# Optimization experiments

Hardware: AMD Instinct MI355X
Metric: run time of the kernel (lower is better)

The kernel has to match this reference:

```python
import jax, jax.numpy as jnp
import numpy as np

B, S, IN_DIM = 4, 2048, 16
D_MODEL, N_HEADS, D_FF = 256, 8, 512
HEAD_DIM = D_MODEL // N_HEADS
EPS = 1e-5


def setup_inputs() -> dict:
    key = jax.random.key(0)
    ks = jax.random.split(key, 16)
    s = 0.02
    return {
        "src": jax.random.normal(ks[0], (B, S, IN_DIM), dtype=jnp.float32),
        "We": jax.random.normal(ks[1], (IN_DIM, D_MODEL), dtype=jnp.float32) * s,
        "be": jnp.zeros((D_MODEL,), jnp.float32),
        "Wq": jax.random.normal(ks[2], (D_MODEL, D_MODEL), dtype=jnp.float32) * s,
        "bq": jnp.zeros((D_MODEL,), jnp.float32),
        "Wk": jax.random.normal(ks[3], (D_MODEL, D_MODEL), dtype=jnp.float32) * s,
        "bk": jnp.zeros((D_MODEL,), jnp.float32),
        "Wv": jax.random.normal(ks[4], (D_MODEL, D_MODEL), dtype=jnp.float32) * s,
        "bv": jnp.zeros((D_MODEL,), jnp.float32),
        "Wo": jax.random.normal(ks[5], (D_MODEL, D_MODEL), dtype=jnp.float32) * s,
        "bo": jnp.zeros((D_MODEL,), jnp.float32),
        "g1": jnp.ones((D_MODEL,), jnp.float32),
        "b1": jnp.zeros((D_MODEL,), jnp.float32),
        "g2": jnp.ones((D_MODEL,), jnp.float32),
        "b2": jnp.zeros((D_MODEL,), jnp.float32),
        "W1": jax.random.normal(ks[6], (D_MODEL, D_FF), dtype=jnp.float32) * s,
        "c1": jnp.zeros((D_FF,), jnp.float32),
        "W2": jax.random.normal(ks[7], (D_FF, D_MODEL), dtype=jnp.float32) * s,
        "c2": jnp.zeros((D_MODEL,), jnp.float32),
    }


def layer_norm(x, g, b):
    mu = jnp.mean(x, axis=-1, keepdims=True)
    var = jnp.mean(jnp.square(x - mu), axis=-1, keepdims=True)
    return (x - mu) * jax.lax.rsqrt(var + EPS) * g + b


def reference(src, We, be, Wq, bq, Wk, bk, Wv, bv, Wo, bo,
              g1, b1, g2, b2, W1, c1, W2, c2):
    # embedding: [B,S,IN] -> [B,S,D]
    emb = src @ We + be
    # projections, split heads: [B,S,D] -> [B,H,S,hd]
    def heads(x):
        return x.reshape(B, S, N_HEADS, HEAD_DIM).transpose(0, 2, 1, 3)
    Q = heads(emb @ Wq + bq)
    K = heads(emb @ Wk + bk)
    V = heads(emb @ Wv + bv)
    scale = jnp.sqrt(jnp.float32(HEAD_DIM))
    energy = jnp.einsum("bhqd,bhkd->bhqk", Q, K) / scale  # [B,H,S,S]
    attn = jax.nn.softmax(energy, axis=-1)
    ctx = jnp.einsum("bhqk,bhkd->bhqd", attn, V)
    ctx = ctx.transpose(0, 2, 1, 3).reshape(B, S, D_MODEL)
    attn_out = ctx @ Wo + bo  # dropout is identity in eval
    x = layer_norm(emb + attn_out, g1, b1)
    ff = jax.nn.relu(x @ W1 + c1) @ W2 + c2
    out = layer_norm(x + ff, g2, b2)
    return out, attn
```

## Files before the change

### kernel.cpp

```cpp
#include <hip/hip_runtime.h>
#include <math.h>

#define SEQ 2048
#define DM 256
#define NH 8
#define HD 32
#define DFF 512
#define BATCH 4
#define NTOK 8192
#define EPS 1e-5f
#define RS 0.17677669529663687f

typedef __attribute__((ext_vector_type(8))) short bf16x8;
typedef __attribute__((ext_vector_type(4))) float f32x4;

#define MFMA16(a, b, c) __builtin_amdgcn_mfma_f32_16x16x32_bf16(a, b, c, 0, 0, 0)

__device__ __forceinline__ unsigned short f2bf(float f) {
    unsigned int u = __float_as_uint(f);
    u = (u + 0x7FFFu + ((u >> 16) & 1u)) >> 16;
    return (unsigned short)u;
}
__device__ __forceinline__ float bf2f(unsigned short h) {
    return __uint_as_float(((unsigned int)h) << 16);
}

__global__ __launch_bounds__(256) void transpose_bf(
    const float* __restrict__ src, unsigned short* __restrict__ dst, int K, int N)
{
    __shared__ float t[16][17];
    const int tx = threadIdx.x & 15, ty = threadIdx.x >> 4;
    const int n0 = blockIdx.x * 16, k0 = blockIdx.y * 16;
    t[ty][tx] = src[(size_t)(k0 + ty) * N + n0 + tx];
    __syncthreads();
    dst[(size_t)(n0 + ty) * K + k0 + tx] = f2bf(t[tx][ty]);
}

__global__ __launch_bounds__(256) void embed_kernel(
    const float* __restrict__ src, const float* __restrict__ We,
    const float* __restrict__ be, float* __restrict__ emb32,
    unsigned short* __restrict__ embb)
{
    __shared__ float s16[16];
    const int row = blockIdx.x, tid = threadIdx.x;
    if (tid < 16) s16[tid] = src[(size_t)row * 16 + tid];
    __syncthreads();
    float acc = be[tid];
    #pragma unroll
    for (int k = 0; k < 16; k++) acc = fmaf(s16[k], We[k * DM + tid], acc);
    emb32[(size_t)row * DM + tid] = acc;
    embb[(size_t)row * DM + tid] = f2bf(acc);
}

template<int OM, bool RELU>
__global__ __launch_bounds__(256) void gemm_bf(
    const unsigned short* __restrict__ A, const unsigned short* __restrict__ Wt,
    const float* __restrict__ bias, void* __restrict__ C, int M, int N, int K)
{
    const int tid = threadIdx.x;
    const int w = tid >> 6, lane = tid & 63;
    const int lo = lane & 15, hi = lane >> 4;
    const int m0 = blockIdx.y * 64 + (w >> 1) * 32;
    const int n0 = blockIdx.x * 64 + (w & 1) * 32;
    f32x4 acc[2][2] = {};
    const unsigned short* Ap0 = A + (size_t)(m0 + lo) * K + hi * 8;
    const unsigned short* Ap1 = Ap0 + (size_t)16 * K;
    const unsigned short* Bp0 = Wt + (size_t)(n0 + lo) * K + hi * 8;
    const unsigned short* Bp1 = Bp0 + (size_t)16 * K;
    for (int k0 = 0; k0 < K; k0 += 32) {
        bf16x8 a0 = *(const bf16x8*)(Ap0 + k0);
        bf16x8 a1 = *(const bf16x8*)(Ap1 + k0);
        bf16x8 b0 = *(const bf16x8*)(Bp0 + k0);
        bf16x8 b1 = *(const bf16x8*)(Bp1 + k0);
        acc[0][0] = MFMA16(a0, b0, acc[0][0]);
        acc[0][1] = MFMA16(a0, b1, acc[0][1]);
        acc[1][0] = MFMA16(a1, b0, acc[1][0]);
        acc[1][1] = MFMA16(a1, b1, acc[1][1]);
    }
    #pragma unroll
    for (int i = 0; i < 2; i++)
        #pragma unroll
        for (int j = 0; j < 2; j++) {
            const int n = n0 + j * 16 + lo;
            const float bz = bias[n];
            #pragma unroll
            for (int r = 0; r < 4; r++) {
                const int m = m0 + i * 16 + 4 * hi + r;
                float v = acc[i][j][r] + bz;
                if (RELU) v = fmaxf(v, 0.f);
                if (OM == 0) {
                    ((float*)C)[(size_t)m * N + n] = v;
                } else if (OM == 1) {
                    ((unsigned short*)C)[(size_t)m * N + n] = f2bf(v);
                } else {
                    const int b = m >> 11, s = m & 2047;
                    const int hh = n >> 5, d = n & 31;
                    ((unsigned short*)C)[((size_t)(b * NH + hh) * HD + d) * SEQ + s] = f2bf(v);
                }
            }
        }
}

__global__ __launch_bounds__(256) void fused_attn(
    const unsigned short* __restrict__ Qb, const unsigned short* __restrict__ Kb,
    const unsigned short* __restrict__ Vt, float* __restrict__ attn,
    unsigned short* __restrict__ ctxb)
{
    __shared__ unsigned short Pt[4][16][40];
    const int tid = threadIdx.x;
    const int w = tid >> 6, lane = tid & 63;
    const int lo = lane & 15, hi = lane >> 4;
    const int bh = blockIdx.y, b = bh >> 3, h = bh & 7;
    const int q0 = blockIdx.x * 64 + w * 16;

    const bf16x8 qf = *(const bf16x8*)(Qb + ((size_t)(b * SEQ) + q0 + lo) * DM + h * HD + hi * 8);
    const unsigned short* Kbase = Kb + (size_t)(b * SEQ) * DM + h * HD + hi * 8;
    const f32x4 zero = {0.f, 0.f, 0.f, 0.f};

    float m[4] = {-3.0e38f, -3.0e38f, -3.0e38f, -3.0e38f};
    float l[4] = {};
    for (int kt = 0; kt < SEQ; kt += 16) {
        bf16x8 kf = *(const bf16x8*)(Kbase + (size_t)(kt + lo) * DM);
        f32x4 s = MFMA16(qf, kf, zero);
        #pragma unroll
        for (int r = 0; r < 4; r++) {
            float v = s[r] * RS;
            float nm = fmaxf(m[r], v);
            l[r] = l[r] * __expf(m[r] - nm) + __expf(v - nm);
            m[r] = nm;
        }
    }
    #pragma unroll
    for (int off = 1; off < 16; off <<= 1) {
        #pragma unroll
        for (int r = 0; r < 4; r++) {
            float m2 = __shfl_xor(m[r], off);
            float l2 = __shfl_xor(l[r], off);
            float M = fmaxf(m[r], m2);
            l[r] = l[r] * __expf(m[r] - M) + l2 * __expf(m2 - M);
            m[r] = M;
        }
    }
    float inv[4];
    #pragma unroll
    for (int r = 0; r < 4; r++) inv[r] = 1.f / l[r];

    f32x4 acc0 = {}, acc1 = {};
    float* attnBase = attn + ((size_t)bh * SEQ + q0) * SEQ;
    const unsigned short* Vtb = Vt + (size_t)bh * HD * SEQ;
    for (int kt = 0; kt < SEQ; kt += 32) {
        #pragma unroll
        for (int sub = 0; sub < 2; sub++) {
            const int k16 = kt + sub * 16;
            bf16x8 kf = *(const bf16x8*)(Kbase + (size_t)(k16 + lo) * DM);
            f32x4 s = MFMA16(qf, kf, zero);
            #pragma unroll
            for (int r = 0; r < 4; r++) {
                float p = __expf(s[r] * RS - m[r]) * inv[r];
                attnBase[(size_t)(4 * hi + r) * SEQ + k16 + lo] = p;
                Pt[w][4 * hi + r][sub * 16 + lo] = f2bf(p);
            }
        }
        __builtin_amdgcn_s_waitcnt(0);
        bf16x8 pa = *(const bf16x8*)&Pt[w][lo][hi * 8];
        bf16x8 v0 = *(const bf16x8*)(Vtb + (size_t)lo * SEQ + kt + hi * 8);
        bf16x8 v1 = *(const bf16x8*)(Vtb + (size_t)(16 + lo) * SEQ + kt + hi * 8);
        acc0 = MFMA16(pa, v0, acc0);
        acc1 = MFMA16(pa, v1, acc1);
    }
    unsigned short* ctxp = ctxb + ((size_t)(b * SEQ) + q0) * DM + h * HD;
    #pragma unroll
    for (int r = 0; r < 4; r++) {
        ctxp[(size_t)(4 * hi + r) * DM + lo]      = f2bf(acc0[r]);
        ctxp[(size_t)(4 * hi + r) * DM + 16 + lo] = f2bf(acc1[r]);
    }
}

template<bool RBF16>
__global__ __launch_bounds__(256) void ln_kernel(
    const float* __restrict__ A, const void* __restrict__ R,
    const float* __restrict__ g, const float* __restrict__ bb,
    float* __restrict__ O32, unsigned short* __restrict__ Ob)
{
    __shared__ float sm[4];
    const size_t row = blockIdx.x;
    const int tid = threadIdx.x;
    float r = RBF16 ? bf2f(((const unsigned short*)R)[row * DM + tid])
                    : ((const float*)R)[row * DM + tid];
    float v = A[row * DM + tid] + r;
    float s = v;
    #pragma unroll
    for (int o = 32; o > 0; o >>= 1) s += __shfl_xor(s, o);
    if ((tid & 63) == 0) sm[tid >> 6] = s;
    __syncthreads();
    s = sm[0] + sm[1] + sm[2] + sm[3];
    __syncthreads();
    float mu = s * (1.f / DM);
    float d = v - mu;
    float s2 = d * d;
    #pragma unroll
    for (int o = 32; o > 0; o >>= 1) s2 += __shfl_xor(s2, o);
    if ((tid & 63) == 0) sm[tid >> 6] = s2;
    __syncthreads();
    s2 = sm[0] + sm[1] + sm[2] + sm[3];
    float rstd = rsqrtf(s2 * (1.f / DM) + EPS);
    float o = d * rstd * g[tid] + bb[tid];
    O32[row * DM + tid] = o;
    if (Ob) Ob[row * DM + tid] = f2bf(o);
}

extern "C" void kernel_launch(void* const* d_in, const int* in_sizes, int n_in,
                              void* d_out, int out_size, void* d_ws, size_t ws_size,
                              hipStream_t stream)
{
    const float* src = (const float*)d_in[0];
    const float* We  = (const float*)d_in[1];
    const float* be  = (const float*)d_in[2];
    const float* Wq  = (const float*)d_in[3];
    const float* bq  = (const float*)d_in[4];
    const float* Wk  = (const float*)d_in[5];
    const float* bk  = (const float*)d_in[6];
    const float* Wv  = (const float*)d_in[7];
    const float* bv  = (const float*)d_in[8];
    const float* Wo  = (const float*)d_in[9];
    const float* bo  = (const float*)d_in[10];
    const float* g1  = (const float*)d_in[11];
    const float* b1  = (const float*)d_in[12];
    const float* g2  = (const float*)d_in[13];
    const float* b2  = (const float*)d_in[14];
    const float* W1  = (const float*)d_in[15];
    const float* c1  = (const float*)d_in[16];
    const float* W2  = (const float*)d_in[17];
    const float* c2  = (const float*)d_in[18];

    float* out  = (float*)d_out;
    float* attn = out + (size_t)NTOK * DM;

    char* ws = (char*)d_ws;
    const size_t MB = 1024 * 1024;
    float*          emb32 = (float*)(ws);
    unsigned short* embb  = (unsigned short*)(ws + 8 * MB);
    unsigned short* Qbf   = (unsigned short*)(ws + 12 * MB);
    unsigned short* Kbf   = (unsigned short*)(ws + 16 * MB);
    unsigned short* Vtb   = (unsigned short*)(ws + 20 * MB);
    unsigned short* Wqt   = (unsigned short*)(ws + 24 * MB);
    unsigned short* Wkt   = (unsigned short*)(ws + 24 * MB + 128 * 1024);
    unsigned short* Wvt   = (unsigned short*)(ws + 24 * MB + 256 * 1024);
    unsigned short* Wot   = (unsigned short*)(ws + 24 * MB + 384 * 1024);
    unsigned short* W1t   = (unsigned short*)(ws + 24 * MB + 512 * 1024);
    unsigned short* W2t   = (unsigned short*)(ws + 24 * MB + 768 * 1024);
    unsigned short* ctxb = embb;
    float*          ao   = (float*)(ws + 12 * MB);
    float*          x32  = emb32;
    unsigned short* xb   = Vtb;
    unsigned short* hb   = (unsigned short*)(ws + 12 * MB);
    unsigned short* ffb  = embb;

    dim3 blk(256);
    transpose_bf<<<dim3(16, 16), blk, 0, stream>>>(Wq, Wqt, DM, DM);
    transpose_bf<<<dim3(16, 16), blk, 0, stream>>>(Wk, Wkt, DM, DM);
    transpose_bf<<<dim3(16, 16), blk, 0, stream>>>(Wv, Wvt, DM, DM);
    transpose_bf<<<dim3(16, 16), blk, 0, stream>>>(Wo, Wot, DM, DM);
    transpose_bf<<<dim3(32, 16), blk, 0, stream>>>(W1, W1t, DM, DFF);
    transpose_bf<<<dim3(16, 32), blk, 0, stream>>>(W2, W2t, DFF, DM);
    embed_kernel<<<dim3(NTOK), blk, 0, stream>>>(src, We, be, emb32, embb);
    gemm_bf<1, false><<<dim3(4, 128), blk, 0, stream>>>(embb, Wqt, bq, Qbf, NTOK, DM, DM);
    gemm_bf<1, false><<<dim3(4, 128), blk, 0, stream>>>(embb, Wkt, bk, Kbf, NTOK, DM, DM);
    gemm_bf<2, false><<<dim3(4, 128), blk, 0, stream>>>(embb, Wvt, bv, Vtb, NTOK, DM, DM);
    fused_attn<<<dim3(SEQ / 64, BATCH * NH), blk, 0, stream>>>(Qbf, Kbf, Vtb, attn, ctxb);
    gemm_bf<0, false><<<dim3(4, 128), blk, 0, stream>>>(ctxb, Wot, bo, ao, NTOK, DM, DM);
    ln_kernel<false><<<dim3(NTOK), blk, 0, stream>>>(emb32, ao, g1, b1, x32, xb);
    gemm_bf<1, true><<<dim3(8, 128), blk, 0, stream>>>(xb, W1t, c1, hb, NTOK, DFF, DM);
    gemm_bf<1, false><<<dim3(4, 128), blk, 0, stream>>>(hb, W2t, c2, ffb, NTOK, DM, DFF);
    ln_kernel<true><<<dim3(NTOK), blk, 0, stream>>>(x32, ffb, g2, b2, out, nullptr);
}
```

Before: 839.9 us.

## Coalesce attention-probability stores via LDS, fuse QKV GEMM, single-exp online softmax

The attention kernel now computes 64 keys per iteration and stages probabilities in shared memory. It writes the attn matrix with float4 stores read back from that staging tile, replacing the scattered scalar stores. The three Q/K/V projections are merged into one launch over a concatenated transposed weight buffer. The first-pass online softmax is rewritten to use one exponential per element instead of two. A side effect is that the stored attention probabilities are now bf16-rounded values widened back to fp32, which lowers output precision.

After: 828.8 us. About the same (-1.3%).

```diff
diff --git a/kernel.cpp b/kernel.cpp
--- a/kernel.cpp
+++ b/kernel.cpp
@@ -13,6 +13,7 @@
 
 typedef __attribute__((ext_vector_type(8))) short bf16x8;
 typedef __attribute__((ext_vector_type(4))) float f32x4;
+typedef __attribute__((ext_vector_type(4))) unsigned short u16x4;
 
 #define MFMA16(a, b, c) __builtin_amdgcn_mfma_f32_16x16x32_bf16(a, b, c, 0, 0, 0)
 
@@ -50,6 +51,58 @@
     for (int k = 0; k < 16; k++) acc = fmaf(s16[k], We[k * DM + tid], acc);
     emb32[(size_t)row * DM + tid] = acc;
     embb[(size_t)row * DM + tid] = f2bf(acc);
+}
+
+__global__ __launch_bounds__(256) void qkv_gemm(
+    const unsigned short* __restrict__ A, const unsigned short* __restrict__ WQKVt,
+    const float* __restrict__ bq, const float* __restrict__ bk,
+    const float* __restrict__ bv,
+    unsigned short* __restrict__ Qb, unsigned short* __restrict__ Kb,
+    unsigned short* __restrict__ Vt)
+{
+    const int tid = threadIdx.x;
+    const int w = tid >> 6, lane = tid & 63;
+    const int lo = lane & 15, hi = lane >> 4;
+    const int which = blockIdx.x >> 2;
+    const float* bias = which == 0 ? bq : (which == 1 ? bk : bv);
+    const int m0 = blockIdx.y * 64 + (w >> 1) * 32;
+    const int n0g = blockIdx.x * 64 + (w & 1) * 32;
+    f32x4 acc[2][2] = {};
+    const unsigned short* Ap0 = A + (size_t)(m0 + lo) * DM + hi * 8;
+    const unsigned short* Ap1 = Ap0 + (size_t)16 * DM;
+    const unsigned short* Bp0 = WQKVt + (size_t)(n0g + lo) * DM + hi * 8;
+    const unsigned short* Bp1 = Bp0 + (size_t)16 * DM;
+    #pragma unroll
+    for (int k0 = 0; k0 < DM; k0 += 32) {
+        bf16x8 a0 = *(const bf16x8*)(Ap0 + k0);
+        bf16x8 a1 = *(const bf16x8*)(Ap1 + k0);
+        bf16x8 b0 = *(const bf16x8*)(Bp0 + k0);
+        bf16x8 b1 = *(const bf16x8*)(Bp1 + k0);
+        acc[0][0] = MFMA16(a0, b0, acc[0][0]);
+        acc[0][1] = MFMA16(a0, b1, acc[0][1]);
+        acc[1][0] = MFMA16(a1, b0, acc[1][0]);
+        acc[1][1] = MFMA16(a1, b1, acc[1][1]);
+    }
+    unsigned short* tok = which == 0 ? Qb : Kb;
+    #pragma unroll
+    for (int i = 0; i < 2; i++)
+        #pragma unroll
+        for (int j = 0; j < 2; j++) {
+            const int nl = (n0g & 255) + j * 16 + lo;
+            const float bz = bias[nl];
+            #pragma unroll
+            for (int r = 0; r < 4; r++) {
+                const int m = m0 + i * 16 + 4 * hi + r;
+                float v = acc[i][j][r] + bz;
+                if (which < 2) {
+                    tok[(size_t)m * DM + nl] = f2bf(v);
+                } else {
+                    const int b = m >> 11, s = m & 2047;
+                    const int hh = nl >> 5, d = nl & 31;
+                    Vt[((size_t)(b * NH + hh) * HD + d) * SEQ + s] = f2bf(v);
+                }
+            }
+        }
 }
 
 template<int OM, bool RELU>
@@ -88,15 +141,8 @@
                 const int m = m0 + i * 16 + 4 * hi + r;
                 float v = acc[i][j][r] + bz;
                 if (RELU) v = fmaxf(v, 0.f);
-                if (OM == 0) {
-                    ((float*)C)[(size_t)m * N + n] = v;
-                } else if (OM == 1) {
-                    ((unsigned short*)C)[(size_t)m * N + n] = f2bf(v);
-                } else {
-                    const int b = m >> 11, s = m & 2047;
-                    const int hh = n >> 5, d = n & 31;
-                    ((unsigned short*)C)[((size_t)(b * NH + hh) * HD + d) * SEQ + s] = f2bf(v);
-                }
+                if (OM == 0) ((float*)C)[(size_t)m * N + n] = v;
+                else         ((unsigned short*)C)[(size_t)m * N + n] = f2bf(v);
             }
         }
 }
@@ -106,7 +152,7 @@
     const unsigned short* __restrict__ Vt, float* __restrict__ attn,
     unsigned short* __restrict__ ctxb)
 {
-    __shared__ unsigned short Pt[4][16][40];
+    __shared__ unsigned short Pt[4][16][72];
     const int tid = threadIdx.x;
     const int w = tid >> 6, lane = tid & 63;
     const int lo = lane & 15, hi = lane >> 4;
@@ -125,9 +171,10 @@
         #pragma unroll
         for (int r = 0; r < 4; r++) {
             float v = s[r] * RS;
-            float nm = fmaxf(m[r], v);
-            l[r] = l[r] * __expf(m[r] - nm) + __expf(v - nm);
-            m[r] = nm;
+            float d = v - m[r];
+            float e = __expf(-fabsf(d));
+            l[r] = d > 0.f ? fmaf(l[r], e, 1.f) : (l[r] + e);
+            m[r] = fmaxf(m[r], v);
         }
     }
     #pragma unroll
@@ -148,25 +195,39 @@
     f32x4 acc0 = {}, acc1 = {};
     float* attnBase = attn + ((size_t)bh * SEQ + q0) * SEQ;
     const unsigned short* Vtb = Vt + (size_t)bh * HD * SEQ;
-    for (int kt = 0; kt < SEQ; kt += 32) {
-        #pragma unroll
-        for (int sub = 0; sub < 2; sub++) {
+    for (int kt = 0; kt < SEQ; kt += 64) {
+        #pragma unroll
+        for (int sub = 0; sub < 4; sub++) {
             const int k16 = kt + sub * 16;
             bf16x8 kf = *(const bf16x8*)(Kbase + (size_t)(k16 + lo) * DM);
             f32x4 s = MFMA16(qf, kf, zero);
             #pragma unroll
             for (int r = 0; r < 4; r++) {
                 float p = __expf(s[r] * RS - m[r]) * inv[r];
-                attnBase[(size_t)(4 * hi + r) * SEQ + k16 + lo] = p;
                 Pt[w][4 * hi + r][sub * 16 + lo] = f2bf(p);
             }
         }
-        __builtin_amdgcn_s_waitcnt(0);
-        bf16x8 pa = *(const bf16x8*)&Pt[w][lo][hi * 8];
-        bf16x8 v0 = *(const bf16x8*)(Vtb + (size_t)lo * SEQ + kt + hi * 8);
-        bf16x8 v1 = *(const bf16x8*)(Vtb + (size_t)(16 + lo) * SEQ + kt + hi * 8);
-        acc0 = MFMA16(pa, v0, acc0);
-        acc1 = MFMA16(pa, v1, acc1);
+        asm volatile("s_waitcnt lgkmcnt(0)" ::: "memory");
+        __builtin_amdgcn_sched_barrier(0);
+        bf16x8 pa0 = *(const bf16x8*)&Pt[w][lo][hi * 8];
+        bf16x8 pa1 = *(const bf16x8*)&Pt[w][lo][32 + hi * 8];
+        bf16x8 v00 = *(const bf16x8*)(Vtb + (size_t)lo * SEQ + kt + hi * 8);
+        bf16x8 v01 = *(const bf16x8*)(Vtb + (size_t)(16 + lo) * SEQ + kt + hi * 8);
+        bf16x8 v10 = *(const bf16x8*)(Vtb + (size_t)lo * SEQ + kt + 32 + hi * 8);
+        bf16x8 v11 = *(const bf16x8*)(Vtb + (size_t)(16 + lo) * SEQ + kt + 32 + hi * 8);
+        acc0 = MFMA16(pa0, v00, acc0);
+        acc1 = MFMA16(pa0, v01, acc1);
+        acc0 = MFMA16(pa1, v10, acc0);
+        acc1 = MFMA16(pa1, v11, acc1);
+        #pragma unroll
+        for (int s4 = 0; s4 < 4; s4++) {
+            const int row = s4 * 4 + hi;
+            const int col = lo * 4;
+            u16x4 u = *(const u16x4*)&Pt[w][row][col];
+            float4 f;
+            f.x = bf2f(u.x); f.y = bf2f(u.y); f.z = bf2f(u.z); f.w = bf2f(u.w);
+            *reinterpret_cast<float4*>(&attnBase[(size_t)row * SEQ + kt + col]) = f;
+        }
     }
     unsigned short* ctxp = ctxb + ((size_t)(b * SEQ) + q0) * DM + h * HD;
     #pragma unroll
@@ -243,7 +304,8 @@
     unsigned short* Qbf   = (unsigned short*)(ws + 12 * MB);
     unsigned short* Kbf   = (unsigned short*)(ws + 16 * MB);
     unsigned short* Vtb   = (unsigned short*)(ws + 20 * MB);
-    unsigned short* Wqt   = (unsigned short*)(ws + 24 * MB);
+    unsigned short* WQKVt = (unsigned short*)(ws + 24 * MB);
+    unsigned short* Wqt   = WQKVt;
     unsigned short* Wkt   = (unsigned short*)(ws + 24 * MB + 128 * 1024);
     unsigned short* Wvt   = (unsigned short*)(ws + 24 * MB + 256 * 1024);
     unsigned short* Wot   = (unsigned short*)(ws + 24 * MB + 384 * 1024);
@@ -264,9 +326,7 @@
     transpose_bf<<<dim3(32, 16), blk, 0, stream>>>(W1, W1t, DM, DFF);
     transpose_bf<<<dim3(16, 32), blk, 0, stream>>>(W2, W2t, DFF, DM);
     embed_kernel<<<dim3(NTOK), blk, 0, stream>>>(src, We, be, emb32, embb);
-    gemm_bf<1, false><<<dim3(4, 128), blk, 0, stream>>>(embb, Wqt, bq, Qbf, NTOK, DM, DM);
-    gemm_bf<1, false><<<dim3(4, 128), blk, 0, stream>>>(embb, Wkt, bk, Kbf, NTOK, DM, DM);
-    gemm_bf<2, false><<<dim3(4, 128), blk, 0, stream>>>(embb, Wvt, bv, Vtb, NTOK, DM, DM);
+    qkv_gemm<<<dim3(12, 128), blk, 0, stream>>>(embb, WQKVt, bq, bk, bv, Qbf, Kbf, Vtb);
     fused_attn<<<dim3(SEQ / 64, BATCH * NH), blk, 0, stream>>>(Qbf, Kbf, Vtb, attn, ctxb);
     gemm_bf<0, false><<<dim3(4, 128), blk, 0, stream>>>(ctxb, Wot, bo, ao, NTOK, DM, DM);
     ln_kernel<false><<<dim3(NTOK), blk, 0, stream>>>(emb32, ao, g1, b1, x32, xb);
```
